# Kernel optimization log

Measured on AMD Instinct MI355X. Metric: run time of the kernel, lower is better.

## Reference

```python
import jax, jax.numpy as jnp
import numpy as np
from jax.ops import segment_sum

N_NODES = 50000


def graph_conv(src, dst, x, W, b, n_nodes):
    # DGL GraphConv with norm='both' (allow_zero_in_degree=True):
    # h = D_in^{-1/2} * A^T (D_out^{-1/2} * x) W + b, degrees clamped to >=1
    ones = jnp.ones(src.shape[0], dtype=x.dtype)
    deg_out = jnp.clip(segment_sum(ones, src, num_segments=n_nodes), 1.0)
    deg_in = jnp.clip(segment_sum(ones, dst, num_segments=n_nodes), 1.0)
    h = x * jax.lax.rsqrt(deg_out)[:, None]
    h = h @ W                      # apply weight before aggregation (mult_W first)
    m = segment_sum(h[src], dst, num_segments=n_nodes)  # sparse neighbor sum
    return m * jax.lax.rsqrt(deg_in)[:, None] + b


def setup_inputs() -> dict:
    key = jax.random.key(0)
    ks = jax.random.split(key, 10)
    n, e = N_NODES, 1600000
    d_in, h1, h2, h3 = 128, 128, 128, 64
    in_feat = jax.random.normal(ks[0], (n, d_in), dtype=jnp.float32)
    src = jax.random.randint(ks[1], (e,), 0, n, dtype=jnp.int32)
    dst = jax.random.randint(ks[2], (e,), 0, n, dtype=jnp.int32)
    s = lambda fi, fo: (1.0 / np.sqrt(fi)).astype(np.float32)
    W1 = jax.random.normal(ks[3], (d_in, h1), dtype=jnp.float32) * s(d_in, h1)
    b1 = jnp.zeros((h1,), dtype=jnp.float32)
    W2 = jax.random.normal(ks[4], (h1, h2), dtype=jnp.float32) * s(h1, h2)
    b2 = jnp.zeros((h2,), dtype=jnp.float32)
    Wf = jax.random.normal(ks[5], (h2, h3), dtype=jnp.float32) * s(h2, h3)
    bf = jnp.zeros((h3,), dtype=jnp.float32)
    return {"in_feat": in_feat, "src": src, "dst": dst,
            "W1": W1, "b1": b1, "W2": W2, "b2": b2, "Wf": Wf, "bf": bf}


def reference(in_feat, src, dst, W1, b1, W2, b2, Wf, bf):
    n = in_feat.shape[0]
    h = graph_conv(src, dst, in_feat, W1, b1, n)
    h = jax.nn.relu(h)
    # dropout(p=0.2) is identity in eval mode
    h = graph_conv(src, dst, h, W2, b2, n)
    return h @ Wf + bf
```

## Files before the change

### kernel.cpp

```cpp
#include <hip/hip_runtime.h>
#include <hip/hip_fp16.h>

#define FD 128
#define OD 64
#define RN 256
#define CHUNKS 256
#define NRMAX 1024

typedef _Float16 f16x8 __attribute__((ext_vector_type(8)));
typedef float    f32x4 __attribute__((ext_vector_type(4)));
typedef float    f32x2 __attribute__((ext_vector_type(2)));


__global__ void prescale_kernel(const float* __restrict__ X, const float* __restrict__ r_out,
                                __half* __restrict__ Xs, int n4) {
    int i = blockIdx.x * 256 + threadIdx.x;
    if (i >= n4) return;
    int v = i >> 5;
    float r = r_out[v];
    float4 t = ((const float4*)X)[i];
    ((__half2*)Xs)[2 * i]     = __floats2half2_rn(t.x * r, t.y * r);
    ((__half2*)Xs)[2 * i + 1] = __floats2half2_rn(t.z * r, t.w * r);
}


__global__ __launch_bounds__(1024) void region_hist_kernel(const int* __restrict__ src,
                                                           const int* __restrict__ dst,
                                                           int* __restrict__ hist_g,
                                                           int* __restrict__ hist_gs,
                                                           int E, int NR, int CS) {
    __shared__ int hist[NRMAX];
    __shared__ int hist_s[NRMAX];
    int c = blockIdx.x;
    for (int t = threadIdx.x; t < NR; t += 1024) { hist[t] = 0; hist_s[t] = 0; }
    __syncthreads();
    int e0 = c * CS, e1 = min(e0 + CS, E);
    int nv = (e1 - e0) & ~3;
    for (int e = e0 + threadIdx.x * 4; e < e0 + nv; e += 4096) {
        int4 d = *(const int4*)(dst + e);
        int4 s = *(const int4*)(src + e);
        atomicAdd(&hist[d.x >> 8], 1);
        atomicAdd(&hist[d.y >> 8], 1);
        atomicAdd(&hist[d.z >> 8], 1);
        atomicAdd(&hist[d.w >> 8], 1);
        atomicAdd(&hist_s[s.x >> 8], 1);
        atomicAdd(&hist_s[s.y >> 8], 1);
        atomicAdd(&hist_s[s.z >> 8], 1);
        atomicAdd(&hist_s[s.w >> 8], 1);
    }
    for (int e = e0 + nv + threadIdx.x; e < e1; e += 1024) {
        atomicAdd(&hist[dst[e] >> 8], 1);
        atomicAdd(&hist_s[src[e] >> 8], 1);
    }
    __syncthreads();
    for (int t = threadIdx.x; t < NR; t += 1024) {
        hist_g[t * CHUNKS + c]  = hist[t];
        hist_gs[t * CHUNKS + c] = hist_s[t];
    }
}

__global__ __launch_bounds__(1024) void region_scan_kernel(const int* __restrict__ hist_g,
                                                           const int* __restrict__ hist_gs,
                                                           int* __restrict__ rstart,
                                                           int* __restrict__ cursor,
                                                           int* __restrict__ sstart,
                                                           int* __restrict__ scursor,
                                                           int NR, int E) {
    __shared__ int wsum[16];
    int tid = threadIdx.x, lane = tid & 63, w = tid >> 6;
    int total = 0;
    if (tid < NR) {
        const int4* hp = (const int4*)(hist_g + (size_t)tid * CHUNKS);
        #pragma unroll 8
        for (int c4 = 0; c4 < CHUNKS / 4; c4++) {
            int4 h = hp[c4];
            total += h.x + h.y + h.z + h.w;
        }
    }
    int x = total;
    #pragma unroll
    for (int d = 1; d < 64; d <<= 1) {
        int t = __shfl_up(x, d, 64);
        if (lane >= d) x += t;
    }
    if (lane == 63) wsum[w] = x;
    __syncthreads();
    if (w == 0) {
        int s = (lane < 16) ? wsum[lane] : 0;
        #pragma unroll
        for (int d = 1; d < 16; d <<= 1) {
            int t = __shfl_up(s, d, 64);
            if (lane >= d) s += t;
        }
        if (lane < 16) wsum[lane] = s;
    }
    __syncthreads();
    int off = (w == 0) ? 0 : wsum[w - 1];
    if (tid < NR) {
        int start = x + off - total;
        rstart[tid] = start;
        int run = start;
        const int4* hp = (const int4*)(hist_g + (size_t)tid * CHUNKS);
        int4* cp = (int4*)(cursor + (size_t)tid * CHUNKS);
        #pragma unroll 8
        for (int c4 = 0; c4 < CHUNKS / 4; c4++) {
            int4 h = hp[c4];
            int4 o;
            o.x = run; run += h.x;
            o.y = run; run += h.y;
            o.z = run; run += h.z;
            o.w = run; run += h.w;
            cp[c4] = o;
        }
    }
    if (tid == 0) rstart[NR] = E;
    __syncthreads();
    total = 0;
    if (tid < NR) {
        const int4* hp = (const int4*)(hist_gs + (size_t)tid * CHUNKS);
        #pragma unroll 8
        for (int c4 = 0; c4 < CHUNKS / 4; c4++) {
            int4 h = hp[c4];
            total += h.x + h.y + h.z + h.w;
        }
    }
    x = total;
    #pragma unroll
    for (int d = 1; d < 64; d <<= 1) {
        int t = __shfl_up(x, d, 64);
        if (lane >= d) x += t;
    }
    if (lane == 63) wsum[w] = x;
    __syncthreads();
    if (w == 0) {
        int s = (lane < 16) ? wsum[lane] : 0;
        #pragma unroll
        for (int d = 1; d < 16; d <<= 1) {
            int t = __shfl_up(s, d, 64);
            if (lane >= d) s += t;
        }
        if (lane < 16) wsum[lane] = s;
    }
    __syncthreads();
    off = (w == 0) ? 0 : wsum[w - 1];
    if (tid < NR) {
        int start = x + off - total;
        sstart[tid] = start;
        int run = start;
        const int4* hp = (const int4*)(hist_gs + (size_t)tid * CHUNKS);
        int4* cp = (int4*)(scursor + (size_t)tid * CHUNKS);
        #pragma unroll 8
        for (int c4 = 0; c4 < CHUNKS / 4; c4++) {
            int4 h = hp[c4];
            int4 o;
            o.x = run; run += h.x;
            o.y = run; run += h.y;
            o.z = run; run += h.z;
            o.w = run; run += h.w;
            cp[c4] = o;
        }
    }
    if (tid == 0) sstart[NR] = E;
}

__global__ __launch_bounds__(1024) void partition_kernel(const int* __restrict__ src,
                                                         const int* __restrict__ dst,
                                                         const int* __restrict__ cursor,
                                                         const int* __restrict__ scursor,
                                                         int* __restrict__ epack,
                                                         unsigned char* __restrict__ spack,
                                                         int E, int NR, int CS) {
    __shared__ int cur[NRMAX];
    __shared__ int scur[NRMAX];
    int c = blockIdx.x;
    for (int t = threadIdx.x; t < NR; t += 1024) {
        cur[t]  = cursor[(size_t)t * CHUNKS + c];
        scur[t] = scursor[(size_t)t * CHUNKS + c];
    }
    __syncthreads();
    int e0 = c * CS, e1 = min(e0 + CS, E);
    int nv = (e1 - e0) & ~3;
    for (int e = e0 + threadIdx.x * 4; e < e0 + nv; e += 4096) {
        int4 d = *(const int4*)(dst + e);
        int4 s = *(const int4*)(src + e);
        int p0 = atomicAdd(&cur[d.x >> 8], 1);
        int p1 = atomicAdd(&cur[d.y >> 8], 1);
        int p2 = atomicAdd(&cur[d.z >> 8], 1);
        int p3 = atomicAdd(&cur[d.w >> 8], 1);
        epack[p0] = ((d.x & 255) << 17) | s.x;
        epack[p1] = ((d.y & 255) << 17) | s.y;
        epack[p2] = ((d.z & 255) << 17) | s.z;
        epack[p3] = ((d.w & 255) << 17) | s.w;
        int q0 = atomicAdd(&scur[s.x >> 8], 1);
        int q1 = atomicAdd(&scur[s.y >> 8], 1);
        int q2 = atomicAdd(&scur[s.z >> 8], 1);
        int q3 = atomicAdd(&scur[s.w >> 8], 1);
        spack[q0] = (unsigned char)(s.x & 255);
        spack[q1] = (unsigned char)(s.y & 255);
        spack[q2] = (unsigned char)(s.z & 255);
        spack[q3] = (unsigned char)(s.w & 255);
    }
    for (int e = e0 + nv + threadIdx.x; e < e1; e += 1024) {
        int d = dst[e], s = src[e];
        int pos = atomicAdd(&cur[d >> 8], 1);
        epack[pos] = ((d & 255) << 17) | s;
        int qos = atomicAdd(&scur[s >> 8], 1);
        spack[qos] = (unsigned char)(s & 255);
    }
}

__global__ __launch_bounds__(1024) void region_sort_kernel(const int* __restrict__ epack,
                                                           const int* __restrict__ rstart,
                                                           int* __restrict__ csrc,
                                                           int* __restrict__ row_start,
                                                           float* __restrict__ r_in,
                                                           int N, int NR, int E) {
    __shared__ int cnt[RN];
    __shared__ int cur[RN];
    __shared__ int wsum[16];
    const int r = blockIdx.x, tid = threadIdx.x;
    const int lane = tid & 63, w = tid >> 6;
    const int s0 = rstart[r], s1 = rstart[r + 1];
    if (tid < RN) cnt[tid] = 0;
    __syncthreads();
    for (int e = s0 + tid; e < s1; e += 1024)
        atomicAdd(&cnt[epack[e] >> 17], 1);
    __syncthreads();
    int cv = (tid < RN) ? cnt[tid] : 0;
    int x = cv;
    #pragma unroll
    for (int d = 1; d < 64; d <<= 1) {
        int t = __shfl_up(x, d, 64);
        if (lane >= d) x += t;
    }
    if (lane == 63 && w < 4) wsum[w] = x;
    __syncthreads();
    if (tid < RN) {
        int woff = 0;
        for (int i = 0; i < w; i++) woff += wsum[i];
        int start = s0 + x - cv + woff;
        cur[tid] = start;
        int node = r * RN + tid;
        if (node < N) {
            row_start[node] = start;
            r_in[node] = rsqrtf((float)max(cv, 1));
        }
    }
    if (r == NR - 1 && tid == 0) row_start[N] = E;
    __syncthreads();
    for (int e = s0 + tid; e < s1; e += 1024) {
        int pk = epack[e];
        int pos = atomicAdd(&cur[pk >> 17], 1);
        csrc[pos] = pk & 0x1FFFF;
    }
}

__global__ __launch_bounds__(256) void rout2_kernel(const unsigned char* __restrict__ spack,
                                                    const int* __restrict__ sstart,
                                                    float* __restrict__ r_out, int N) {
    __shared__ int cnt[RN];
    const int r = blockIdx.x, tid = threadIdx.x;
    const int s0 = sstart[r], s1 = sstart[r + 1];
    cnt[tid] = 0;
    __syncthreads();
    for (int e = s0 + tid; e < s1; e += 256)
        atomicAdd(&cnt[spack[e]], 1);
    __syncthreads();
    int node = r * RN + tid;
    if (node < N) r_out[node] = rsqrtf((float)max(cnt[tid], 1));
}

__global__ __launch_bounds__(256) void agg128_kernel(const __half* __restrict__ Xs,
                                                     const float* __restrict__ r_in,
                                                     const int* __restrict__ rs,
                                                     const int* __restrict__ csrc,
                                                     __half* __restrict__ Z, int N) {
    const int lane = threadIdx.x & 63, wv = threadIdx.x >> 6;
    int v = blockIdx.x * 4 + wv;
    if (v >= N) return;
    int s0 = __builtin_amdgcn_readfirstlane(rs[v]);
    int s1 = __builtin_amdgcn_readfirstlane(rs[v + 1]);
    const int deg = s1 - s0;
    float ax = 0.f, ay = 0.f;
    const int nb = deg >> 4;
    int e = s0;
    if (nb) {
        int ia[16];
        #pragma unroll
        for (int u = 0; u < 16; u++) ia[u] = __builtin_nontemporal_load(csrc + e + u);
        for (int b = 1; b < nb; b++) {
            __half2 t[16];
            #pragma unroll
            for (int u = 0; u < 16; u++)
                t[u] = ((const __half2*)(Xs + (size_t)ia[u] * FD))[lane];
            int eb = e + (b << 4);
            #pragma unroll
            for (int u = 0; u < 16; u++) ia[u] = __builtin_nontemporal_load(csrc + eb + u);
            #pragma unroll
            for (int u = 0; u < 16; u++) {
                float2 f = __half22float2(t[u]);
                ax += f.x; ay += f.y;
            }
        }
        __half2 t[16];
        #pragma unroll
        for (int u = 0; u < 16; u++)
            t[u] = ((const __half2*)(Xs + (size_t)ia[u] * FD))[lane];
        #pragma unroll
        for (int u = 0; u < 16; u++) {
            float2 f = __half22float2(t[u]);
            ax += f.x; ay += f.y;
        }
        e += nb << 4;
    }
    const int rem = s1 - e;
    if (rem) {
        const int last = s1 - 1;
        int ia[16];
        #pragma unroll
        for (int u = 0; u < 16; u++)
            ia[u] = __builtin_nontemporal_load(csrc + min(e + u, last));
        #pragma unroll
        for (int u = 0; u < 16; u++) {
            unsigned raw = ((const unsigned*)(Xs + (size_t)ia[u] * FD))[lane];
            raw = (u < rem) ? raw : 0u;
            union { unsigned q; __half2 h; } tt; tt.q = raw;
            float2 f = __half22float2(tt.h);
            ax += f.x; ay += f.y;
        }
    }
    float ri = r_in[v];
    union { __half2 h; unsigned q; } o;
    o.h = __floats2half2_rn(ax * ri, ay * ri);
    __builtin_nontemporal_store(o.q, (unsigned*)(Z + (size_t)v * FD) + lane);
}

__global__ __launch_bounds__(256) void agg64_kernel(const __half* __restrict__ T,
                                                    const float* __restrict__ r_in,
                                                    const int* __restrict__ rs,
                                                    const int* __restrict__ csrc,
                                                    const float* __restrict__ bc,
                                                    float* __restrict__ out, int N) {
    const int tid = threadIdx.x;
    const int lane = tid & 63, wv = tid >> 6;
    const int hf = lane >> 5, l32 = lane & 31;
    int v = blockIdx.x * 8 + wv * 2 + hf;
    if (v >= N) return;
    int s0 = rs[v], s1 = rs[v + 1];
    const int deg = s1 - s0;
    float ax = 0.f, ay = 0.f;
    const int nb = deg >> 3;
    int e = s0;
    if (nb) {
        int ia[8];
        #pragma unroll
        for (int u = 0; u < 8; u++) ia[u] = __builtin_nontemporal_load(csrc + e + u);
        for (int b = 1; b < nb; b++) {
            __half2 t[8];
            #pragma unroll
            for (int u = 0; u < 8; u++)
                t[u] = ((const __half2*)(T + (size_t)ia[u] * OD))[l32];
            int eb = e + (b << 3);
            #pragma unroll
            for (int u = 0; u < 8; u++) ia[u] = __builtin_nontemporal_load(csrc + eb + u);
            #pragma unroll
            for (int u = 0; u < 8; u++) {
                float2 f = __half22float2(t[u]);
                ax += f.x; ay += f.y;
            }
        }
        __half2 t[8];
        #pragma unroll
        for (int u = 0; u < 8; u++)
            t[u] = ((const __half2*)(T + (size_t)ia[u] * OD))[l32];
        #pragma unroll
        for (int u = 0; u < 8; u++) {
            float2 f = __half22float2(t[u]);
            ax += f.x; ay += f.y;
        }
        e += nb << 3;
    }
    const int rem = s1 - e;
    if (rem) {
        const int last = s1 - 1;
        int ia[8];
        #pragma unroll
        for (int u = 0; u < 8; u++)
            ia[u] = __builtin_nontemporal_load(csrc + min(e + u, last));
        #pragma unroll
        for (int u = 0; u < 8; u++) {
            unsigned raw = ((const unsigned*)(T + (size_t)ia[u] * OD))[l32];
            raw = (u < rem) ? raw : 0u;
            union { unsigned q; __half2 h; } tt; tt.q = raw;
            float2 f = __half22float2(tt.h);
            ax += f.x; ay += f.y;
        }
    }
    float ri = r_in[v];
    f32x2 o;
    o.x = ax * ri + bc[l32 * 2];
    o.y = ay * ri + bc[l32 * 2 + 1];
    __builtin_nontemporal_store(o, (f32x2*)(out + (size_t)v * OD) + l32);
}

__global__ __launch_bounds__(256) void gemm1_mfma_kernel(const __half* __restrict__ Ah,
                                                         const __half* __restrict__ Bh,
                                                         const float* __restrict__ b1,
                                                         const float* __restrict__ rowscale,
                                                         __half* __restrict__ Ch,
                                                         int M, int ntiles) {
    const int w = threadIdx.x >> 6, lane = threadIdx.x & 63;
    const int l15 = lane & 15, quad = lane >> 4;
    const _Float16* B = (const _Float16*)Bh;

    f16x8 bfrag[2][4];
    #pragma unroll
    for (int nt = 0; nt < 2; nt++) {
        int col = 32 * w + 16 * nt + l15;
        #pragma unroll
        for (int kk = 0; kk < 4; kk++) {
            int kb = kk * 32 + quad * 8;
            f16x8 bf;
            #pragma unroll
            for (int j = 0; j < 8; j++) bf[j] = B[(size_t)(kb + j) * FD + col];
            bfrag[nt][kk] = bf;
        }
    }

    for (int t = blockIdx.x; t < ntiles; t += gridDim.x) {
        int row0 = t * 16;
        const _Float16* Arow = (const _Float16*)Ah + (size_t)(row0 + l15) * FD + quad * 8;
        f16x8 afrag[4];
        #pragma unroll
        for (int kk = 0; kk < 4; kk++) afrag[kk] = *(const f16x8*)(Arow + kk * 32);
        f32x4 acc0 = {0.f, 0.f, 0.f, 0.f};
        f32x4 acc1 = {0.f, 0.f, 0.f, 0.f};
        #pragma unroll
        for (int kk = 0; kk < 4; kk++) {
            acc0 = __builtin_amdgcn_mfma_f32_16x16x32_f16(afrag[kk], bfrag[0][kk], acc0, 0, 0, 0);
            acc1 = __builtin_amdgcn_mfma_f32_16x16x32_f16(afrag[kk], bfrag[1][kk], acc1, 0, 0, 0);
        }
        int c0 = 32 * w + l15, c1 = c0 + 16;
        float bb0 = b1[c0], bb1 = b1[c1];
        #pragma unroll
        for (int r = 0; r < 4; r++) {
            int row = row0 + quad * 4 + r;
            if (row < M) {
                float rsc = rowscale[row];
                Ch[(size_t)row * FD + c0] = __float2half(fmaxf(acc0[r] + bb0, 0.f) * rsc);
                Ch[(size_t)row * FD + c1] = __float2half(fmaxf(acc1[r] + bb1, 0.f) * rsc);
            }
        }
    }
}

__global__ __launch_bounds__(256) void gemm2_mfma_kernel(const __half* __restrict__ Ah,
                                                         const __half* __restrict__ Bh,
                                                         __half* __restrict__ Ch,
                                                         int M, int ntiles) {
    const int w = threadIdx.x >> 6, lane = threadIdx.x & 63;
    const int l15 = lane & 15, quad = lane >> 4;
    const _Float16* B = (const _Float16*)Bh;

    f16x8 bfrag[4];
    int col = 16 * w + l15;
    #pragma unroll
    for (int kk = 0; kk < 4; kk++) {
        int kb = kk * 32 + quad * 8;
        f16x8 bf;
        #pragma unroll
        for (int j = 0; j < 8; j++) bf[j] = B[(size_t)(kb + j) * OD + col];
        bfrag[kk] = bf;
    }

    for (int t = blockIdx.x; t < ntiles; t += gridDim.x) {
        int row0 = t * 16;
        const _Float16* Arow = (const _Float16*)Ah + (size_t)(row0 + l15) * FD + quad * 8;
        f16x8 afrag[4];
        #pragma unroll
        for (int kk = 0; kk < 4; kk++) afrag[kk] = *(const f16x8*)(Arow + kk * 32);
        f32x4 acc = {0.f, 0.f, 0.f, 0.f};
        #pragma unroll
        for (int kk = 0; kk < 4; kk++)
            acc = __builtin_amdgcn_mfma_f32_16x16x32_f16(afrag[kk], bfrag[kk], acc, 0, 0, 0);
        #pragma unroll
        for (int r = 0; r < 4; r++) {
            int row = row0 + quad * 4 + r;
            if (row < M)
                Ch[(size_t)row * OD + col] = __float2half(acc[r]);
        }
    }
}

__global__ void fold_kernel(const float* __restrict__ W2, const float* __restrict__ Wf,
                            const float* __restrict__ b2, const float* __restrict__ bf,
                            const float* __restrict__ W1,
                            __half* __restrict__ W1h, __half* __restrict__ Wch,
                            float* __restrict__ bc) {
    int idx = blockIdx.x * 256 + threadIdx.x;
    if (idx < FD * FD) W1h[idx] = __float2half(W1[idx]);
    if (idx < FD * OD) {
        int i = idx / OD, j = idx % OD;
        float s = 0.f;
        for (int k = 0; k < FD; k++) s += W2[i * FD + k] * Wf[k * OD + j];
        Wch[idx] = __float2half(s);
    }
    if (idx < OD) {
        float s = bf[idx];
        for (int k = 0; k < FD; k++) s += b2[k] * Wf[k * OD + idx];
        bc[idx] = s;
    }
}

extern "C" void kernel_launch(void* const* d_in, const int* in_sizes, int n_in,
                              void* d_out, int out_size, void* d_ws, size_t ws_size,
                              hipStream_t stream) {
    const float* in_feat = (const float*)d_in[0];
    const int*   src     = (const int*)d_in[1];
    const int*   dst     = (const int*)d_in[2];
    const float* W1      = (const float*)d_in[3];
    const float* b1      = (const float*)d_in[4];
    const float* W2      = (const float*)d_in[5];
    const float* b2      = (const float*)d_in[6];
    const float* Wf      = (const float*)d_in[7];
    const float* bf      = (const float*)d_in[8];
    float* out = (float*)d_out;

    const int N = in_sizes[0] / FD;
    const int E = in_sizes[1];
    const int NR = (N + RN - 1) / RN;
    const int CS = (((E + CHUNKS - 1) / CHUNKS) + 3) & ~3;

    char* ws = (char*)d_ws;
    size_t off = 0;
    auto alloc = [&](size_t bytes) -> void* {
        void* p = ws + off;
        off += (bytes + 255) / 256 * 256;
        return p;
    };
    unsigned char* spack = (unsigned char*)alloc((size_t)E);
    int*    epack   = (int*)alloc((size_t)E * 4);
    __half* tbuf    = (__half*)spack;
    float*  r_out   = (float*)alloc((size_t)N * 4);
    float*  r_in    = (float*)alloc((size_t)N * 4);
    int*    hist_g  = (int*)alloc((size_t)CHUNKS * NRMAX * 4);
    int*    hist_gs = (int*)alloc((size_t)CHUNKS * NRMAX * 4);
    int*    cursor  = (int*)alloc((size_t)CHUNKS * NRMAX * 4);
    int*    scursor = (int*)alloc((size_t)CHUNKS * NRMAX * 4);
    int*    rstart  = (int*)alloc((size_t)(NR + 1) * 4);
    int*    sstart  = (int*)alloc((size_t)(NR + 1) * 4);
    int*    csrc    = (int*)alloc((size_t)E * 4);
    int*    row_start = (int*)alloc((size_t)(N + 1) * 4);
    __half* z1h     = (__half*)alloc((size_t)N * FD * 2);
    __half* y1h     = (__half*)alloc((size_t)N * FD * 2);
    __half* Xs      = (__half*)alloc((size_t)N * FD * 2);
    __half* W1h     = (__half*)alloc((size_t)FD * FD * 2);
    __half* Wch     = (__half*)alloc((size_t)FD * OD * 2);
    float*  bc      = (float*)alloc((size_t)OD * 4);
    (void)ws_size; (void)n_in; (void)out_size;

    const int ntiles = (N + 15) / 16;
    const int gemmgrid = ntiles < 1024 ? ntiles : 1024;

    region_hist_kernel<<<CHUNKS, 1024, 0, stream>>>(src, dst, hist_g, hist_gs, E, NR, CS);
    region_scan_kernel<<<1, 1024, 0, stream>>>(hist_g, hist_gs, rstart, cursor, sstart, scursor, NR, E);
    partition_kernel<<<CHUNKS, 1024, 0, stream>>>(src, dst, cursor, scursor, epack, spack, E, NR, CS);
    region_sort_kernel<<<NR, 1024, 0, stream>>>(epack, rstart, csrc, row_start, r_in, N, NR, E);
    rout2_kernel<<<NR, 256, 0, stream>>>(spack, sstart, r_out, N);

    fold_kernel<<<(FD * FD + 255) / 256, 256, 0, stream>>>(W2, Wf, b2, bf, W1, W1h, Wch, bc);

    prescale_kernel<<<(N * 32 + 255) / 256, 256, 0, stream>>>(in_feat, r_out, Xs, N * 32);
    agg128_kernel<<<(N + 3) / 4, 256, 0, stream>>>(Xs, r_in, row_start, csrc, z1h, N);

    gemm1_mfma_kernel<<<gemmgrid, 256, 0, stream>>>(z1h, W1h, b1, r_out, y1h, N, ntiles);
    gemm2_mfma_kernel<<<gemmgrid, 256, 0, stream>>>(y1h, Wch, tbuf, N, ntiles);

    agg64_kernel<<<(N + 7) / 8, 256, 0, stream>>>(tbuf, r_in, row_start, csrc, bc, out, N);
}
```

Measured before the change: 287.0 us.

## Fuse first aggregation with both GEMMs and compute out-degree via global atomics

The layer-1 neighbor aggregation, the W1 GEMM with bias/ReLU/scale, and the folded W2·Wf GEMM now run in one kernel. Each block aggregates 16 rows into shared memory and runs the MFMAs there, so the z1 and y1 intermediates no longer go through global memory. Out-degree is now counted with per-node global atomics instead of a second region histogram, scan, partition and count pass. The csrc loads also drop their nontemporal hints. The cost is contended global atomics on 50k counters and lower occupancy from the shared tiles and the per-block B-fragment loads.

```diff
diff --git a/kernel.cpp b/kernel.cpp
--- a/kernel.cpp
+++ b/kernel.cpp
@@ -11,6 +11,16 @@
 typedef float    f32x4 __attribute__((ext_vector_type(4)));
 typedef float    f32x2 __attribute__((ext_vector_type(2)));
 
+
+__global__ void zero_deg_kernel(int* __restrict__ deg, int N) {
+    int i = blockIdx.x * 256 + threadIdx.x;
+    if (i < N) deg[i] = 0;
+}
+
+__global__ void rout_kernel(const int* __restrict__ deg, float* __restrict__ r_out, int N) {
+    int i = blockIdx.x * 256 + threadIdx.x;
+    if (i < N) r_out[i] = rsqrtf((float)max(deg[i], 1));
+}
 
 __global__ void prescale_kernel(const float* __restrict__ X, const float* __restrict__ r_out,
                                 __half* __restrict__ Xs, int n4) {
@@ -27,12 +37,11 @@
 __global__ __launch_bounds__(1024) void region_hist_kernel(const int* __restrict__ src,
                                                            const int* __restrict__ dst,
                                                            int* __restrict__ hist_g,
-                                                           int* __restrict__ hist_gs,
+                                                           int* __restrict__ deg_out,
                                                            int E, int NR, int CS) {
     __shared__ int hist[NRMAX];
-    __shared__ int hist_s[NRMAX];
     int c = blockIdx.x;
-    for (int t = threadIdx.x; t < NR; t += 1024) { hist[t] = 0; hist_s[t] = 0; }
+    for (int t = threadIdx.x; t < NR; t += 1024) hist[t] = 0;
     __syncthreads();
     int e0 = c * CS, e1 = min(e0 + CS, E);
     int nv = (e1 - e0) & ~3;
@@ -43,28 +52,23 @@
         atomicAdd(&hist[d.y >> 8], 1);
         atomicAdd(&hist[d.z >> 8], 1);
         atomicAdd(&hist[d.w >> 8], 1);
-        atomicAdd(&hist_s[s.x >> 8], 1);
-        atomicAdd(&hist_s[s.y >> 8], 1);
-        atomicAdd(&hist_s[s.z >> 8], 1);
-        atomicAdd(&hist_s[s.w >> 8], 1);
+        atomicAdd(&deg_out[s.x], 1);
+        atomicAdd(&deg_out[s.y], 1);
+        atomicAdd(&deg_out[s.z], 1);
+        atomicAdd(&deg_out[s.w], 1);
     }
     for (int e = e0 + nv + threadIdx.x; e < e1; e += 1024) {
         atomicAdd(&hist[dst[e] >> 8], 1);
-        atomicAdd(&hist_s[src[e] >> 8], 1);
-    }
-    __syncthreads();
-    for (int t = threadIdx.x; t < NR; t += 1024) {
-        hist_g[t * CHUNKS + c]  = hist[t];
-        hist_gs[t * CHUNKS + c] = hist_s[t];
-    }
+        atomicAdd(&deg_out[src[e]], 1);
+    }
+    __syncthreads();
+    for (int t = threadIdx.x; t < NR; t += 1024)
+        hist_g[t * CHUNKS + c] = hist[t];
 }
 
 __global__ __launch_bounds__(1024) void region_scan_kernel(const int* __restrict__ hist_g,
-                                                           const int* __restrict__ hist_gs,
                                                            int* __restrict__ rstart,
                                                            int* __restrict__ cursor,
-                                                           int* __restrict__ sstart,
-                                                           int* __restrict__ scursor,
                                                            int NR, int E) {
     __shared__ int wsum[16];
     int tid = threadIdx.x, lane = tid & 63, w = tid >> 6;
@@ -114,69 +118,17 @@
         }
     }
     if (tid == 0) rstart[NR] = E;
-    __syncthreads();
-    total = 0;
-    if (tid < NR) {
-        const int4* hp = (const int4*)(hist_gs + (size_t)tid * CHUNKS);
-        #pragma unroll 8
-        for (int c4 = 0; c4 < CHUNKS / 4; c4++) {
-            int4 h = hp[c4];
-            total += h.x + h.y + h.z + h.w;
-        }
-    }
-    x = total;
-    #pragma unroll
-    for (int d = 1; d < 64; d <<= 1) {
-        int t = __shfl_up(x, d, 64);
-        if (lane >= d) x += t;
-    }
-    if (lane == 63) wsum[w] = x;
-    __syncthreads();
-    if (w == 0) {
-        int s = (lane < 16) ? wsum[lane] : 0;
-        #pragma unroll
-        for (int d = 1; d < 16; d <<= 1) {
-            int t = __shfl_up(s, d, 64);
-            if (lane >= d) s += t;
-        }
-        if (lane < 16) wsum[lane] = s;
-    }
-    __syncthreads();
-    off = (w == 0) ? 0 : wsum[w - 1];
-    if (tid < NR) {
-        int start = x + off - total;
-        sstart[tid] = start;
-        int run = start;
-        const int4* hp = (const int4*)(hist_gs + (size_t)tid * CHUNKS);
-        int4* cp = (int4*)(scursor + (size_t)tid * CHUNKS);
-        #pragma unroll 8
-        for (int c4 = 0; c4 < CHUNKS / 4; c4++) {
-            int4 h = hp[c4];
-            int4 o;
-            o.x = run; run += h.x;
-            o.y = run; run += h.y;
-            o.z = run; run += h.z;
-            o.w = run; run += h.w;
-            cp[c4] = o;
-        }
-    }
-    if (tid == 0) sstart[NR] = E;
 }
 
 __global__ __launch_bounds__(1024) void partition_kernel(const int* __restrict__ src,
                                                          const int* __restrict__ dst,
                                                          const int* __restrict__ cursor,
-                                                         const int* __restrict__ scursor,
                                                          int* __restrict__ epack,
-                                                         unsigned char* __restrict__ spack,
                                                          int E, int NR, int CS) {
     __shared__ int cur[NRMAX];
-    __shared__ int scur[NRMAX];
     int c = blockIdx.x;
-    for (int t = threadIdx.x; t < NR; t += 1024) {
-        cur[t]  = cursor[(size_t)t * CHUNKS + c];
-        scur[t] = scursor[(size_t)t * CHUNKS + c];
-    }
+    for (int t = threadIdx.x; t < NR; t += 1024)
+        cur[t] = cursor[(size_t)t * CHUNKS + c];
     __syncthreads();
     int e0 = c * CS, e1 = min(e0 + CS, E);
     int nv = (e1 - e0) & ~3;
@@ -191,21 +143,11 @@
         epack[p1] = ((d.y & 255) << 17) | s.y;
         epack[p2] = ((d.z & 255) << 17) | s.z;
         epack[p3] = ((d.w & 255) << 17) | s.w;
-        int q0 = atomicAdd(&scur[s.x >> 8], 1);
-        int q1 = atomicAdd(&scur[s.y >> 8], 1);
-        int q2 = atomicAdd(&scur[s.z >> 8], 1);
-        int q3 = atomicAdd(&scur[s.w >> 8], 1);
-        spack[q0] = (unsigned char)(s.x & 255);
-        spack[q1] = (unsigned char)(s.y & 255);
-        spack[q2] = (unsigned char)(s.z & 255);
-        spack[q3] = (unsigned char)(s.w & 255);
     }
     for (int e = e0 + nv + threadIdx.x; e < e1; e += 1024) {
         int d = dst[e], s = src[e];
         int pos = atomicAdd(&cur[d >> 8], 1);
         epack[pos] = ((d & 255) << 17) | s;
-        int qos = atomicAdd(&scur[s >> 8], 1);
-        spack[qos] = (unsigned char)(s & 255);
     }
 }
 
@@ -255,84 +197,153 @@
     }
 }
 
-__global__ __launch_bounds__(256) void rout2_kernel(const unsigned char* __restrict__ spack,
-                                                    const int* __restrict__ sstart,
-                                                    float* __restrict__ r_out, int N) {
-    __shared__ int cnt[RN];
-    const int r = blockIdx.x, tid = threadIdx.x;
-    const int s0 = sstart[r], s1 = sstart[r + 1];
-    cnt[tid] = 0;
-    __syncthreads();
-    for (int e = s0 + tid; e < s1; e += 256)
-        atomicAdd(&cnt[spack[e]], 1);
-    __syncthreads();
-    int node = r * RN + tid;
-    if (node < N) r_out[node] = rsqrtf((float)max(cnt[tid], 1));
-}
-
-__global__ __launch_bounds__(256) void agg128_kernel(const __half* __restrict__ Xs,
+__global__ __launch_bounds__(256) void fused1_kernel(const __half* __restrict__ Xs,
                                                      const float* __restrict__ r_in,
+                                                     const float* __restrict__ r_out,
                                                      const int* __restrict__ rs,
                                                      const int* __restrict__ csrc,
-                                                     __half* __restrict__ Z, int N) {
-    const int lane = threadIdx.x & 63, wv = threadIdx.x >> 6;
-    int v = blockIdx.x * 4 + wv;
-    if (v >= N) return;
-    int s0 = __builtin_amdgcn_readfirstlane(rs[v]);
-    int s1 = __builtin_amdgcn_readfirstlane(rs[v + 1]);
-    const int deg = s1 - s0;
-    float ax = 0.f, ay = 0.f;
-    const int nb = deg >> 4;
-    int e = s0;
-    if (nb) {
-        int ia[16];
-        #pragma unroll
-        for (int u = 0; u < 16; u++) ia[u] = __builtin_nontemporal_load(csrc + e + u);
-        for (int b = 1; b < nb; b++) {
-            __half2 t[16];
+                                                     const __half* __restrict__ W1h,
+                                                     const float* __restrict__ b1,
+                                                     const __half* __restrict__ Wch,
+                                                     __half* __restrict__ tbuf,
+                                                     int N) {
+    const int tid = threadIdx.x;
+    const int lane = tid & 63, w = tid >> 6;
+    const int l15 = lane & 15, quad = lane >> 4;
+    const int base = blockIdx.x * 16;
+    __shared__ __half2  zt[16][68];
+    __shared__ _Float16 yt[16][136];
+
+    for (int j = 0; j < 4; j++) {
+        const int row = 4 * j + w;
+        const int v = base + row;
+        float ax = 0.f, ay = 0.f;
+        if (v < N) {
+            int s0 = __builtin_amdgcn_readfirstlane(rs[v]);
+            int s1 = __builtin_amdgcn_readfirstlane(rs[v + 1]);
+            const int deg = s1 - s0;
+            const int nb = deg >> 4;
+            int e = s0;
+            if (nb) {
+                int ia[16];
+                #pragma unroll
+                for (int u = 0; u < 16; u++) ia[u] = csrc[e + u];
+                for (int b = 1; b < nb; b++) {
+                    __half2 t[16];
+                    #pragma unroll
+                    for (int u = 0; u < 16; u++)
+                        t[u] = ((const __half2*)(Xs + (size_t)ia[u] * FD))[lane];
+                    int eb = e + (b << 4);
+                    #pragma unroll
+                    for (int u = 0; u < 16; u++) ia[u] = csrc[eb + u];
+                    #pragma unroll
+                    for (int u = 0; u < 16; u++) {
+                        float2 f = __half22float2(t[u]);
+                        ax += f.x; ay += f.y;
+                    }
+                }
+                __half2 t[16];
+                #pragma unroll
+                for (int u = 0; u < 16; u++)
+                    t[u] = ((const __half2*)(Xs + (size_t)ia[u] * FD))[lane];
+                #pragma unroll
+                for (int u = 0; u < 16; u++) {
+                    float2 f = __half22float2(t[u]);
+                    ax += f.x; ay += f.y;
+                }
+                e += nb << 4;
+            }
+            const int rem = s1 - e;
+            if (rem) {
+                const int last = s1 - 1;
+                int ia[16];
+                #pragma unroll
+                for (int u = 0; u < 16; u++) ia[u] = csrc[min(e + u, last)];
+                #pragma unroll
+                for (int u = 0; u < 16; u++) {
+                    unsigned raw = ((const unsigned*)(Xs + (size_t)ia[u] * FD))[lane];
+                    raw = (u < rem) ? raw : 0u;
+                    union { unsigned q; __half2 h; } tt; tt.q = raw;
+                    float2 f = __half22float2(tt.h);
+                    ax += f.x; ay += f.y;
+                }
+            }
+            float ri = r_in[v];
+            zt[row][lane] = __floats2half2_rn(ax * ri, ay * ri);
+        } else {
+            zt[row][lane] = __floats2half2_rn(0.f, 0.f);
+        }
+    }
+    __syncthreads();
+
+    const _Float16* B1 = (const _Float16*)W1h;
+    const _Float16* B2 = (const _Float16*)Wch;
+    f16x8 bf1[2][4];
+    #pragma unroll
+    for (int nt = 0; nt < 2; nt++) {
+        int col = 32 * w + 16 * nt + l15;
+        #pragma unroll
+        for (int kk = 0; kk < 4; kk++) {
+            int kb = kk * 32 + quad * 8;
+            f16x8 bf;
             #pragma unroll
-            for (int u = 0; u < 16; u++)
-                t[u] = ((const __half2*)(Xs + (size_t)ia[u] * FD))[lane];
-            int eb = e + (b << 4);
-            #pragma unroll
-            for (int u = 0; u < 16; u++) ia[u] = __builtin_nontemporal_load(csrc + eb + u);
-            #pragma unroll
-            for (int u = 0; u < 16; u++) {
-                float2 f = __half22float2(t[u]);
-                ax += f.x; ay += f.y;
-            }
-        }
-        __half2 t[16];
-        #pragma unroll
-        for (int u = 0; u < 16; u++)
-            t[u] = ((const __half2*)(Xs + (size_t)ia[u] * FD))[lane];
-        #pragma unroll
-        for (int u = 0; u < 16; u++) {
-            float2 f = __half22float2(t[u]);
-            ax += f.x; ay += f.y;
-        }
-        e += nb << 4;
-    }
-    const int rem = s1 - e;
-    if (rem) {
-        const int last = s1 - 1;
-        int ia[16];
-        #pragma unroll
-        for (int u = 0; u < 16; u++)
-            ia[u] = __builtin_nontemporal_load(csrc + min(e + u, last));
-        #pragma unroll
-        for (int u = 0; u < 16; u++) {
-            unsigned raw = ((const unsigned*)(Xs + (size_t)ia[u] * FD))[lane];
-            raw = (u < rem) ? raw : 0u;
-            union { unsigned q; __half2 h; } tt; tt.q = raw;
-            float2 f = __half22float2(tt.h);
-            ax += f.x; ay += f.y;
-        }
-    }
-    float ri = r_in[v];
-    union { __half2 h; unsigned q; } o;
-    o.h = __floats2half2_rn(ax * ri, ay * ri);
-    __builtin_nontemporal_store(o.q, (unsigned*)(Z + (size_t)v * FD) + lane);
+            for (int j = 0; j < 8; j++) bf[j] = B1[(size_t)(kb + j) * FD + col];
+            bf1[nt][kk] = bf;
+        }
+    }
+    f16x8 bf2[4];
+    const int col2 = 16 * w + l15;
+    #pragma unroll
+    for (int kk = 0; kk < 4; kk++) {
+        int kb = kk * 32 + quad * 8;
+        f16x8 bf;
+        #pragma unroll
+        for (int j = 0; j < 8; j++) bf[j] = B2[(size_t)(kb + j) * OD + col2];
+        bf2[kk] = bf;
+    }
+
+    {
+        const _Float16* Arow = (const _Float16*)&zt[l15][0] + quad * 8;
+        f16x8 afrag[4];
+        #pragma unroll
+        for (int kk = 0; kk < 4; kk++) afrag[kk] = *(const f16x8*)(Arow + kk * 32);
+        f32x4 acc0 = {0.f, 0.f, 0.f, 0.f};
+        f32x4 acc1 = {0.f, 0.f, 0.f, 0.f};
+        #pragma unroll
+        for (int kk = 0; kk < 4; kk++) {
+            acc0 = __builtin_amdgcn_mfma_f32_16x16x32_f16(afrag[kk], bf1[0][kk], acc0, 0, 0, 0);
+            acc1 = __builtin_amdgcn_mfma_f32_16x16x32_f16(afrag[kk], bf1[1][kk], acc1, 0, 0, 0);
+        }
+        int c0 = 32 * w + l15, c1 = c0 + 16;
+        float bb0 = b1[c0], bb1 = b1[c1];
+        #pragma unroll
+        for (int r = 0; r < 4; r++) {
+            int row = quad * 4 + r;
+            int v = base + row;
+            float rsc = (v < N) ? r_out[v] : 0.f;
+            yt[row][c0] = (_Float16)(fmaxf(acc0[r] + bb0, 0.f) * rsc);
+            yt[row][c1] = (_Float16)(fmaxf(acc1[r] + bb1, 0.f) * rsc);
+        }
+    }
+    __syncthreads();
+
+    {
+        const _Float16* Arow = &yt[l15][0] + quad * 8;
+        f16x8 afrag[4];
+        #pragma unroll
+        for (int kk = 0; kk < 4; kk++) afrag[kk] = *(const f16x8*)(Arow + kk * 32);
+        f32x4 acc = {0.f, 0.f, 0.f, 0.f};
+        #pragma unroll
+        for (int kk = 0; kk < 4; kk++)
+            acc = __builtin_amdgcn_mfma_f32_16x16x32_f16(afrag[kk], bf2[kk], acc, 0, 0, 0);
+        #pragma unroll
+        for (int r = 0; r < 4; r++) {
+            int row = quad * 4 + r;
+            int v = base + row;
+            if (v < N)
+                tbuf[(size_t)v * OD + col2] = __float2half(acc[r]);
+        }
+    }
 }
 
 __global__ __launch_bounds__(256) void agg64_kernel(const __half* __restrict__ T,
@@ -354,7 +365,7 @@
     if (nb) {
         int ia[8];
         #pragma unroll
-        for (int u = 0; u < 8; u++) ia[u] = __builtin_nontemporal_load(csrc + e + u);
+        for (int u = 0; u < 8; u++) ia[u] = csrc[e + u];
         for (int b = 1; b < nb; b++) {
             __half2 t[8];
             #pragma unroll
@@ -362,7 +373,7 @@
                 t[u] = ((const __half2*)(T + (size_t)ia[u] * OD))[l32];
             int eb = e + (b << 3);
             #pragma unroll
-            for (int u = 0; u < 8; u++) ia[u] = __builtin_nontemporal_load(csrc + eb + u);
+            for (int u = 0; u < 8; u++) ia[u] = csrc[eb + u];
             #pragma unroll
             for (int u = 0; u < 8; u++) {
                 float2 f = __half22float2(t[u]);
@@ -385,8 +396,7 @@
         const int last = s1 - 1;
         int ia[8];
         #pragma unroll
-        for (int u = 0; u < 8; u++)
-            ia[u] = __builtin_nontemporal_load(csrc + min(e + u, last));
+        for (int u = 0; u < 8; u++) ia[u] = csrc[min(e + u, last)];
         #pragma unroll
         for (int u = 0; u < 8; u++) {
             unsigned raw = ((const unsigned*)(T + (size_t)ia[u] * OD))[l32];
@@ -401,95 +411,6 @@
     o.x = ax * ri + bc[l32 * 2];
     o.y = ay * ri + bc[l32 * 2 + 1];
     __builtin_nontemporal_store(o, (f32x2*)(out + (size_t)v * OD) + l32);
-}
-
-__global__ __launch_bounds__(256) void gemm1_mfma_kernel(const __half* __restrict__ Ah,
-                                                         const __half* __restrict__ Bh,
-                                                         const float* __restrict__ b1,
-                                                         const float* __restrict__ rowscale,
-                                                         __half* __restrict__ Ch,
-                                                         int M, int ntiles) {
-    const int w = threadIdx.x >> 6, lane = threadIdx.x & 63;
-    const int l15 = lane & 15, quad = lane >> 4;
-    const _Float16* B = (const _Float16*)Bh;
-
-    f16x8 bfrag[2][4];
-    #pragma unroll
-    for (int nt = 0; nt < 2; nt++) {
-        int col = 32 * w + 16 * nt + l15;
-        #pragma unroll
-        for (int kk = 0; kk < 4; kk++) {
-            int kb = kk * 32 + quad * 8;
-            f16x8 bf;
-            #pragma unroll
-            for (int j = 0; j < 8; j++) bf[j] = B[(size_t)(kb + j) * FD + col];
-            bfrag[nt][kk] = bf;
-        }
-    }
-
-    for (int t = blockIdx.x; t < ntiles; t += gridDim.x) {
-        int row0 = t * 16;
-        const _Float16* Arow = (const _Float16*)Ah + (size_t)(row0 + l15) * FD + quad * 8;
-        f16x8 afrag[4];
-        #pragma unroll
-        for (int kk = 0; kk < 4; kk++) afrag[kk] = *(const f16x8*)(Arow + kk * 32);
-        f32x4 acc0 = {0.f, 0.f, 0.f, 0.f};
-        f32x4 acc1 = {0.f, 0.f, 0.f, 0.f};
-        #pragma unroll
-        for (int kk = 0; kk < 4; kk++) {
-            acc0 = __builtin_amdgcn_mfma_f32_16x16x32_f16(afrag[kk], bfrag[0][kk], acc0, 0, 0, 0);
-            acc1 = __builtin_amdgcn_mfma_f32_16x16x32_f16(afrag[kk], bfrag[1][kk], acc1, 0, 0, 0);
-        }
-        int c0 = 32 * w + l15, c1 = c0 + 16;
-        float bb0 = b1[c0], bb1 = b1[c1];
-        #pragma unroll
-        for (int r = 0; r < 4; r++) {
-            int row = row0 + quad * 4 + r;
-            if (row < M) {
-                float rsc = rowscale[row];
-                Ch[(size_t)row * FD + c0] = __float2half(fmaxf(acc0[r] + bb0, 0.f) * rsc);
-                Ch[(size_t)row * FD + c1] = __float2half(fmaxf(acc1[r] + bb1, 0.f) * rsc);
-            }
-        }
-    }
-}
-
-__global__ __launch_bounds__(256) void gemm2_mfma_kernel(const __half* __restrict__ Ah,
-                                                         const __half* __restrict__ Bh,
-                                                         __half* __restrict__ Ch,
-                                                         int M, int ntiles) {
-    const int w = threadIdx.x >> 6, lane = threadIdx.x & 63;
-    const int l15 = lane & 15, quad = lane >> 4;
-    const _Float16* B = (const _Float16*)Bh;
-
-    f16x8 bfrag[4];
-    int col = 16 * w + l15;
-    #pragma unroll
-    for (int kk = 0; kk < 4; kk++) {
-        int kb = kk * 32 + quad * 8;
-        f16x8 bf;
-        #pragma unroll
-        for (int j = 0; j < 8; j++) bf[j] = B[(size_t)(kb + j) * OD + col];
-        bfrag[kk] = bf;
-    }
-
-    for (int t = blockIdx.x; t < ntiles; t += gridDim.x) {
-        int row0 = t * 16;
-        const _Float16* Arow = (const _Float16*)Ah + (size_t)(row0 + l15) * FD + quad * 8;
-        f16x8 afrag[4];
-        #pragma unroll
-        for (int kk = 0; kk < 4; kk++) afrag[kk] = *(const f16x8*)(Arow + kk * 32);
-        f32x4 acc = {0.f, 0.f, 0.f, 0.f};
-        #pragma unroll
-        for (int kk = 0; kk < 4; kk++)
-            acc = __builtin_amdgcn_mfma_f32_16x16x32_f16(afrag[kk], bfrag[kk], acc, 0, 0, 0);
-        #pragma unroll
-        for (int r = 0; r < 4; r++) {
-            int row = row0 + quad * 4 + r;
-            if (row < M)
-                Ch[(size_t)row * OD + col] = __float2half(acc[r]);
-        }
-    }
 }
 
 __global__ void fold_kernel(const float* __restrict__ W2, const float* __restrict__ Wf,
@@ -538,43 +459,36 @@
         off += (bytes + 255) / 256 * 256;
         return p;
     };
-    unsigned char* spack = (unsigned char*)alloc((size_t)E);
     int*    epack   = (int*)alloc((size_t)E * 4);
-    __half* tbuf    = (__half*)spack;
+    __half* tbuf    = (__half*)epack;
     float*  r_out   = (float*)alloc((size_t)N * 4);
     float*  r_in    = (float*)alloc((size_t)N * 4);
+    int*    deg_out = (int*)alloc((size_t)N * 4);
     int*    hist_g  = (int*)alloc((size_t)CHUNKS * NRMAX * 4);
-    int*    hist_gs = (int*)alloc((size_t)CHUNKS * NRMAX * 4);
     int*    cursor  = (int*)alloc((size_t)CHUNKS * NRMAX * 4);
-    int*    scursor = (int*)alloc((size_t)CHUNKS * NRMAX * 4);
     int*    rstart  = (int*)alloc((size_t)(NR + 1) * 4);
-    int*    sstart  = (int*)alloc((size_t)(NR + 1) * 4);
     int*    csrc    = (int*)alloc((size_t)E * 4);
     int*    row_start = (int*)alloc((size_t)(N + 1) * 4);
-    __half* z1h     = (__half*)alloc((size_t)N * FD * 2);
-    __half* y1h     = (__half*)alloc((size_t)N * FD * 2);
     __half* Xs      = (__half*)alloc((size_t)N * FD * 2);
     __half* W1h     = (__half*)alloc((size_t)FD * FD * 2);
     __half* Wch     = (__half*)alloc((size_t)FD * OD * 2);
     float*  bc      = (float*)alloc((size_t)OD * 4);
     (void)ws_size; (void)n_in; (void)out_size;
 
-    const int ntiles = (N + 15) / 16;
-    const int gemmgrid = ntiles < 1024 ? ntiles : 1024;
-
-    region_hist_kernel<<<CHUNKS, 1024, 0, stream>>>(src, dst, hist_g, hist_gs, E, NR, CS);
-    region_scan_kernel<<<1, 1024, 0, stream>>>(hist_g, hist_gs, rstart, cursor, sstart, scursor, NR, E);
-    partition_kernel<<<CHUNKS, 1024, 0, stream>>>(src, dst, cursor, scursor, epack, spack, E, NR, CS);
+    const int nblk = (N + 255) / 256;
+
+    zero_deg_kernel<<<nblk, 256, 0, stream>>>(deg_out, N);
+    region_hist_kernel<<<CHUNKS, 1024, 0, stream>>>(src, dst, hist_g, deg_out, E, NR, CS);
+    region_scan_kernel<<<1, 1024, 0, stream>>>(hist_g, rstart, cursor, NR, E);
+    partition_kernel<<<CHUNKS, 1024, 0, stream>>>(src, dst, cursor, epack, E, NR, CS);
     region_sort_kernel<<<NR, 1024, 0, stream>>>(epack, rstart, csrc, row_start, r_in, N, NR, E);
-    rout2_kernel<<<NR, 256, 0, stream>>>(spack, sstart, r_out, N);
+    rout_kernel<<<nblk, 256, 0, stream>>>(deg_out, r_out, N);
 
     fold_kernel<<<(FD * FD + 255) / 256, 256, 0, stream>>>(W2, Wf, b2, bf, W1, W1h, Wch, bc);
 
     prescale_kernel<<<(N * 32 + 255) / 256, 256, 0, stream>>>(in_feat, r_out, Xs, N * 32);
-    agg128_kernel<<<(N + 3) / 4, 256, 0, stream>>>(Xs, r_in, row_start, csrc, z1h, N);
-
-    gemm1_mfma_kernel<<<gemmgrid, 256, 0, stream>>>(z1h, W1h, b1, r_out, y1h, N, ntiles);
-    gemm2_mfma_kernel<<<gemmgrid, 256, 0, stream>>>(y1h, Wch, tbuf, N, ntiles);
+    fused1_kernel<<<(N + 15) / 16, 256, 0, stream>>>(Xs, r_in, r_out, row_start, csrc,
+                                                     W1h, b1, Wch, tbuf, N);
 
     agg64_kernel<<<(N + 7) / 8, 256, 0, stream>>>(tbuf, r_in, row_start, csrc, bc, out, N);
 }
```

New measurement: 305.4 us. 6.4% more time.

## Fuse first aggregation with both MFMA GEMMs through shared-memory tiles

Applied to the files above, without the earlier changes.

Replaces the separate 128-wide aggregation kernel and the two MFMA GEMM kernels with one kernel. Each block aggregates 16 nodes into an LDS tile, runs the first GEMM with bias, ReLU and row scaling into a second LDS tile, then runs the folded second GEMM and writes the 64-wide intermediate. This removes two launches and the global round trips of the z1 and y1 buffers. In exchange, every block reloads the weight fragments from global memory and adds barriers, and the smaller per-block work may cost occupancy or latency hiding. Nontemporal index loads are also switched to ordinary loads.

```diff
diff --git a/kernel.cpp b/kernel.cpp
--- a/kernel.cpp
+++ b/kernel.cpp
@@ -270,69 +270,153 @@
     if (node < N) r_out[node] = rsqrtf((float)max(cnt[tid], 1));
 }
 
-__global__ __launch_bounds__(256) void agg128_kernel(const __half* __restrict__ Xs,
+__global__ __launch_bounds__(256) void fused1_kernel(const __half* __restrict__ Xs,
                                                      const float* __restrict__ r_in,
+                                                     const float* __restrict__ r_out,
                                                      const int* __restrict__ rs,
                                                      const int* __restrict__ csrc,
-                                                     __half* __restrict__ Z, int N) {
-    const int lane = threadIdx.x & 63, wv = threadIdx.x >> 6;
-    int v = blockIdx.x * 4 + wv;
-    if (v >= N) return;
-    int s0 = __builtin_amdgcn_readfirstlane(rs[v]);
-    int s1 = __builtin_amdgcn_readfirstlane(rs[v + 1]);
-    const int deg = s1 - s0;
-    float ax = 0.f, ay = 0.f;
-    const int nb = deg >> 4;
-    int e = s0;
-    if (nb) {
-        int ia[16];
-        #pragma unroll
-        for (int u = 0; u < 16; u++) ia[u] = __builtin_nontemporal_load(csrc + e + u);
-        for (int b = 1; b < nb; b++) {
-            __half2 t[16];
+                                                     const __half* __restrict__ W1h,
+                                                     const float* __restrict__ b1,
+                                                     const __half* __restrict__ Wch,
+                                                     __half* __restrict__ tbuf,
+                                                     int N) {
+    const int tid = threadIdx.x;
+    const int lane = tid & 63, w = tid >> 6;
+    const int l15 = lane & 15, quad = lane >> 4;
+    const int base = blockIdx.x * 16;
+    __shared__ __half2  zt[16][68];
+    __shared__ _Float16 yt[16][136];
+
+    for (int j = 0; j < 4; j++) {
+        const int row = 4 * j + w;
+        const int v = base + row;
+        float ax = 0.f, ay = 0.f;
+        if (v < N) {
+            int s0 = __builtin_amdgcn_readfirstlane(rs[v]);
+            int s1 = __builtin_amdgcn_readfirstlane(rs[v + 1]);
+            const int deg = s1 - s0;
+            const int nb = deg >> 4;
+            int e = s0;
+            if (nb) {
+                int ia[16];
+                #pragma unroll
+                for (int u = 0; u < 16; u++) ia[u] = csrc[e + u];
+                for (int b = 1; b < nb; b++) {
+                    __half2 t[16];
+                    #pragma unroll
+                    for (int u = 0; u < 16; u++)
+                        t[u] = ((const __half2*)(Xs + (size_t)ia[u] * FD))[lane];
+                    int eb = e + (b << 4);
+                    #pragma unroll
+                    for (int u = 0; u < 16; u++) ia[u] = csrc[eb + u];
+                    #pragma unroll
+                    for (int u = 0; u < 16; u++) {
+                        float2 f = __half22float2(t[u]);
+                        ax += f.x; ay += f.y;
+                    }
+                }
+                __half2 t[16];
+                #pragma unroll
+                for (int u = 0; u < 16; u++)
+                    t[u] = ((const __half2*)(Xs + (size_t)ia[u] * FD))[lane];
+                #pragma unroll
+                for (int u = 0; u < 16; u++) {
+                    float2 f = __half22float2(t[u]);
+                    ax += f.x; ay += f.y;
+                }
+                e += nb << 4;
+            }
+            const int rem = s1 - e;
+            if (rem) {
+                const int last = s1 - 1;
+                int ia[16];
+                #pragma unroll
+                for (int u = 0; u < 16; u++) ia[u] = csrc[min(e + u, last)];
+                #pragma unroll
+                for (int u = 0; u < 16; u++) {
+                    unsigned raw = ((const unsigned*)(Xs + (size_t)ia[u] * FD))[lane];
+                    raw = (u < rem) ? raw : 0u;
+                    union { unsigned q; __half2 h; } tt; tt.q = raw;
+                    float2 f = __half22float2(tt.h);
+                    ax += f.x; ay += f.y;
+                }
+            }
+            float ri = r_in[v];
+            zt[row][lane] = __floats2half2_rn(ax * ri, ay * ri);
+        } else {
+            zt[row][lane] = __floats2half2_rn(0.f, 0.f);
+        }
+    }
+    __syncthreads();
+
+    const _Float16* B1 = (const _Float16*)W1h;
+    const _Float16* B2 = (const _Float16*)Wch;
+    f16x8 bf1[2][4];
+    #pragma unroll
+    for (int nt = 0; nt < 2; nt++) {
+        int col = 32 * w + 16 * nt + l15;
+        #pragma unroll
+        for (int kk = 0; kk < 4; kk++) {
+            int kb = kk * 32 + quad * 8;
+            f16x8 bf;
             #pragma unroll
-            for (int u = 0; u < 16; u++)
-                t[u] = ((const __half2*)(Xs + (size_t)ia[u] * FD))[lane];
-            int eb = e + (b << 4);
-            #pragma unroll
-            for (int u = 0; u < 16; u++) ia[u] = __builtin_nontemporal_load(csrc + eb + u);
-            #pragma unroll
-            for (int u = 0; u < 16; u++) {
-                float2 f = __half22float2(t[u]);
-                ax += f.x; ay += f.y;
-            }
-        }
-        __half2 t[16];
-        #pragma unroll
-        for (int u = 0; u < 16; u++)
-            t[u] = ((const __half2*)(Xs + (size_t)ia[u] * FD))[lane];
-        #pragma unroll
-        for (int u = 0; u < 16; u++) {
-            float2 f = __half22float2(t[u]);
-            ax += f.x; ay += f.y;
-        }
-        e += nb << 4;
-    }
-    const int rem = s1 - e;
-    if (rem) {
-        const int last = s1 - 1;
-        int ia[16];
-        #pragma unroll
-        for (int u = 0; u < 16; u++)
-            ia[u] = __builtin_nontemporal_load(csrc + min(e + u, last));
-        #pragma unroll
-        for (int u = 0; u < 16; u++) {
-            unsigned raw = ((const unsigned*)(Xs + (size_t)ia[u] * FD))[lane];
-            raw = (u < rem) ? raw : 0u;
-            union { unsigned q; __half2 h; } tt; tt.q = raw;
-            float2 f = __half22float2(tt.h);
-            ax += f.x; ay += f.y;
-        }
-    }
-    float ri = r_in[v];
-    union { __half2 h; unsigned q; } o;
-    o.h = __floats2half2_rn(ax * ri, ay * ri);
-    __builtin_nontemporal_store(o.q, (unsigned*)(Z + (size_t)v * FD) + lane);
+            for (int j = 0; j < 8; j++) bf[j] = B1[(size_t)(kb + j) * FD + col];
+            bf1[nt][kk] = bf;
+        }
+    }
+    f16x8 bf2[4];
+    const int col2 = 16 * w + l15;
+    #pragma unroll
+    for (int kk = 0; kk < 4; kk++) {
+        int kb = kk * 32 + quad * 8;
+        f16x8 bf;
+        #pragma unroll
+        for (int j = 0; j < 8; j++) bf[j] = B2[(size_t)(kb + j) * OD + col2];
+        bf2[kk] = bf;
+    }
+
+    {
+        const _Float16* Arow = (const _Float16*)&zt[l15][0] + quad * 8;
+        f16x8 afrag[4];
+        #pragma unroll
+        for (int kk = 0; kk < 4; kk++) afrag[kk] = *(const f16x8*)(Arow + kk * 32);
+        f32x4 acc0 = {0.f, 0.f, 0.f, 0.f};
+        f32x4 acc1 = {0.f, 0.f, 0.f, 0.f};
+        #pragma unroll
+        for (int kk = 0; kk < 4; kk++) {
+            acc0 = __builtin_amdgcn_mfma_f32_16x16x32_f16(afrag[kk], bf1[0][kk], acc0, 0, 0, 0);
+            acc1 = __builtin_amdgcn_mfma_f32_16x16x32_f16(afrag[kk], bf1[1][kk], acc1, 0, 0, 0);
+        }
+        int c0 = 32 * w + l15, c1 = c0 + 16;
+        float bb0 = b1[c0], bb1 = b1[c1];
+        #pragma unroll
+        for (int r = 0; r < 4; r++) {
+            int row = quad * 4 + r;
+            int v = base + row;
+            float rsc = (v < N) ? r_out[v] : 0.f;
+            yt[row][c0] = (_Float16)(fmaxf(acc0[r] + bb0, 0.f) * rsc);
+            yt[row][c1] = (_Float16)(fmaxf(acc1[r] + bb1, 0.f) * rsc);
+        }
+    }
+    __syncthreads();
+
+    {
+        const _Float16* Arow = &yt[l15][0] + quad * 8;
+        f16x8 afrag[4];
+        #pragma unroll
+        for (int kk = 0; kk < 4; kk++) afrag[kk] = *(const f16x8*)(Arow + kk * 32);
+        f32x4 acc = {0.f, 0.f, 0.f, 0.f};
+        #pragma unroll
+        for (int kk = 0; kk < 4; kk++)
+            acc = __builtin_amdgcn_mfma_f32_16x16x32_f16(afrag[kk], bf2[kk], acc, 0, 0, 0);
+        #pragma unroll
+        for (int r = 0; r < 4; r++) {
+            int row = quad * 4 + r;
+            int v = base + row;
+            if (v < N)
+                tbuf[(size_t)v * OD + col2] = __float2half(acc[r]);
+        }
+    }
 }
 
 __global__ __launch_bounds__(256) void agg64_kernel(const __half* __restrict__ T,
@@ -354,7 +438,7 @@
     if (nb) {
         int ia[8];
         #pragma unroll
-        for (int u = 0; u < 8; u++) ia[u] = __builtin_nontemporal_load(csrc + e + u);
+        for (int u = 0; u < 8; u++) ia[u] = csrc[e + u];
         for (int b = 1; b < nb; b++) {
             __half2 t[8];
             #pragma unroll
@@ -362,7 +446,7 @@
                 t[u] = ((const __half2*)(T + (size_t)ia[u] * OD))[l32];
             int eb = e + (b << 3);
             #pragma unroll
-            for (int u = 0; u < 8; u++) ia[u] = __builtin_nontemporal_load(csrc + eb + u);
+            for (int u = 0; u < 8; u++) ia[u] = csrc[eb + u];
             #pragma unroll
             for (int u = 0; u < 8; u++) {
                 float2 f = __half22float2(t[u]);
@@ -385,8 +469,7 @@
         const int last = s1 - 1;
         int ia[8];
         #pragma unroll
-        for (int u = 0; u < 8; u++)
-            ia[u] = __builtin_nontemporal_load(csrc + min(e + u, last));
+        for (int u = 0; u < 8; u++) ia[u] = csrc[min(e + u, last)];
         #pragma unroll
         for (int u = 0; u < 8; u++) {
             unsigned raw = ((const unsigned*)(T + (size_t)ia[u] * OD))[l32];
@@ -401,95 +484,6 @@
     o.x = ax * ri + bc[l32 * 2];
     o.y = ay * ri + bc[l32 * 2 + 1];
     __builtin_nontemporal_store(o, (f32x2*)(out + (size_t)v * OD) + l32);
-}
-
-__global__ __launch_bounds__(256) void gemm1_mfma_kernel(const __half* __restrict__ Ah,
-                                                         const __half* __restrict__ Bh,
-                                                         const float* __restrict__ b1,
-                                                         const float* __restrict__ rowscale,
-                                                         __half* __restrict__ Ch,
-                                                         int M, int ntiles) {
-    const int w = threadIdx.x >> 6, lane = threadIdx.x & 63;
-    const int l15 = lane & 15, quad = lane >> 4;
-    const _Float16* B = (const _Float16*)Bh;
-
-    f16x8 bfrag[2][4];
-    #pragma unroll
-    for (int nt = 0; nt < 2; nt++) {
-        int col = 32 * w + 16 * nt + l15;
-        #pragma unroll
-        for (int kk = 0; kk < 4; kk++) {
-            int kb = kk * 32 + quad * 8;
-            f16x8 bf;
-            #pragma unroll
-            for (int j = 0; j < 8; j++) bf[j] = B[(size_t)(kb + j) * FD + col];
-            bfrag[nt][kk] = bf;
-        }
-    }
-
-    for (int t = blockIdx.x; t < ntiles; t += gridDim.x) {
-        int row0 = t * 16;
-        const _Float16* Arow = (const _Float16*)Ah + (size_t)(row0 + l15) * FD + quad * 8;
-        f16x8 afrag[4];
-        #pragma unroll
-        for (int kk = 0; kk < 4; kk++) afrag[kk] = *(const f16x8*)(Arow + kk * 32);
-        f32x4 acc0 = {0.f, 0.f, 0.f, 0.f};
-        f32x4 acc1 = {0.f, 0.f, 0.f, 0.f};
-        #pragma unroll
-        for (int kk = 0; kk < 4; kk++) {
-            acc0 = __builtin_amdgcn_mfma_f32_16x16x32_f16(afrag[kk], bfrag[0][kk], acc0, 0, 0, 0);
-            acc1 = __builtin_amdgcn_mfma_f32_16x16x32_f16(afrag[kk], bfrag[1][kk], acc1, 0, 0, 0);
-        }
-        int c0 = 32 * w + l15, c1 = c0 + 16;
-        float bb0 = b1[c0], bb1 = b1[c1];
-        #pragma unroll
-        for (int r = 0; r < 4; r++) {
-            int row = row0 + quad * 4 + r;
-            if (row < M) {
-                float rsc = rowscale[row];
-                Ch[(size_t)row * FD + c0] = __float2half(fmaxf(acc0[r] + bb0, 0.f) * rsc);
-                Ch[(size_t)row * FD + c1] = __float2half(fmaxf(acc1[r] + bb1, 0.f) * rsc);
-            }
-        }
-    }
-}
-
-__global__ __launch_bounds__(256) void gemm2_mfma_kernel(const __half* __restrict__ Ah,
-                                                         const __half* __restrict__ Bh,
-                                                         __half* __restrict__ Ch,
-                                                         int M, int ntiles) {
-    const int w = threadIdx.x >> 6, lane = threadIdx.x & 63;
-    const int l15 = lane & 15, quad = lane >> 4;
-    const _Float16* B = (const _Float16*)Bh;
-
-    f16x8 bfrag[4];
-    int col = 16 * w + l15;
-    #pragma unroll
-    for (int kk = 0; kk < 4; kk++) {
-        int kb = kk * 32 + quad * 8;
-        f16x8 bf;
-        #pragma unroll
-        for (int j = 0; j < 8; j++) bf[j] = B[(size_t)(kb + j) * OD + col];
-        bfrag[kk] = bf;
-    }
-
-    for (int t = blockIdx.x; t < ntiles; t += gridDim.x) {
-        int row0 = t * 16;
-        const _Float16* Arow = (const _Float16*)Ah + (size_t)(row0 + l15) * FD + quad * 8;
-        f16x8 afrag[4];
-        #pragma unroll
-        for (int kk = 0; kk < 4; kk++) afrag[kk] = *(const f16x8*)(Arow + kk * 32);
-        f32x4 acc = {0.f, 0.f, 0.f, 0.f};
-        #pragma unroll
-        for (int kk = 0; kk < 4; kk++)
-            acc = __builtin_amdgcn_mfma_f32_16x16x32_f16(afrag[kk], bfrag[kk], acc, 0, 0, 0);
-        #pragma unroll
-        for (int r = 0; r < 4; r++) {
-            int row = row0 + quad * 4 + r;
-            if (row < M)
-                Ch[(size_t)row * OD + col] = __float2half(acc[r]);
-        }
-    }
 }
 
 __global__ void fold_kernel(const float* __restrict__ W2, const float* __restrict__ Wf,
@@ -551,17 +545,12 @@
     int*    sstart  = (int*)alloc((size_t)(NR + 1) * 4);
     int*    csrc    = (int*)alloc((size_t)E * 4);
     int*    row_start = (int*)alloc((size_t)(N + 1) * 4);
-    __half* z1h     = (__half*)alloc((size_t)N * FD * 2);
-    __half* y1h     = (__half*)alloc((size_t)N * FD * 2);
     __half* Xs      = (__half*)alloc((size_t)N * FD * 2);
     __half* W1h     = (__half*)alloc((size_t)FD * FD * 2);
     __half* Wch     = (__half*)alloc((size_t)FD * OD * 2);
     float*  bc      = (float*)alloc((size_t)OD * 4);
     (void)ws_size; (void)n_in; (void)out_size;
 
-    const int ntiles = (N + 15) / 16;
-    const int gemmgrid = ntiles < 1024 ? ntiles : 1024;
-
     region_hist_kernel<<<CHUNKS, 1024, 0, stream>>>(src, dst, hist_g, hist_gs, E, NR, CS);
     region_scan_kernel<<<1, 1024, 0, stream>>>(hist_g, hist_gs, rstart, cursor, sstart, scursor, NR, E);
     partition_kernel<<<CHUNKS, 1024, 0, stream>>>(src, dst, cursor, scursor, epack, spack, E, NR, CS);
@@ -571,10 +560,8 @@
     fold_kernel<<<(FD * FD + 255) / 256, 256, 0, stream>>>(W2, Wf, b2, bf, W1, W1h, Wch, bc);
 
     prescale_kernel<<<(N * 32 + 255) / 256, 256, 0, stream>>>(in_feat, r_out, Xs, N * 32);
-    agg128_kernel<<<(N + 3) / 4, 256, 0, stream>>>(Xs, r_in, row_start, csrc, z1h, N);
-
-    gemm1_mfma_kernel<<<gemmgrid, 256, 0, stream>>>(z1h, W1h, b1, r_out, y1h, N, ntiles);
-    gemm2_mfma_kernel<<<gemmgrid, 256, 0, stream>>>(y1h, Wch, tbuf, N, ntiles);
+    fused1_kernel<<<(N + 15) / 16, 256, 0, stream>>>(Xs, r_in, r_out, row_start, csrc,
+                                                     W1h, b1, Wch, tbuf, N);
 
     agg64_kernel<<<(N + 7) / 8, 256, 0, stream>>>(tbuf, r_in, row_start, csrc, bc, out, N);
 }
```

New measurement: 276.4 us. -3.7%, faster.
